# Optimization experiments

Measured on AMD Instinct MI355X. Metric: run time of the kernel, lower is better.

The kernel has to match this reference:

```python
import jax, jax.numpy as jnp
import numpy as np

CL = 128   # context_length
IL = 64    # inst_length
PC = 256; CH1 = 256; CH2 = 256; CH3 = 256
CK1 = 3; CK2 = 3; CK3 = 3
F1 = 512; OUT = 1
F1_INPUT = CH3 * (CL - 1 - CK1 - CK2 - CK3 + 3)  # 256*121 = 30976
B = 2048


def _conv1d(x, w, b):
    # x: [B, Cin, L], w: [Cout, Cin, K] -> [B, Cout, L-K+1]
    y = jax.lax.conv_general_dilated(x, w, window_strides=(1,), padding='VALID',
                                     dimension_numbers=('NCH', 'OIH', 'NCH'))
    return y + b[None, :, None]


def setup_inputs() -> dict:
    key = jax.random.key(0)
    ks = jax.random.split(key, 13)
    def w(k, shape, fan_in):
        bound = 1.0 / np.sqrt(fan_in)
        return jax.random.uniform(k, shape, jnp.float32, -bound, bound)
    return {
        'x':   jax.random.normal(ks[0], (B, CL * IL), jnp.float32),
        'Wp':  w(ks[1], (PC, IL, 2), IL * 2),
        'bp':  w(ks[2], (PC,), IL * 2),
        'W1':  w(ks[3], (CH1, PC, CK1), PC * CK1),
        'b1':  w(ks[4], (CH1,), PC * CK1),
        'W2':  w(ks[5], (CH2, CH1, CK2), CH1 * CK2),
        'b2':  w(ks[6], (CH2,), CH1 * CK2),
        'W3':  w(ks[7], (CH3, CH2, CK3), CH2 * CK3),
        'b3':  w(ks[8], (CH3,), CH2 * CK3),
        'Wf1': w(ks[9], (F1, F1_INPUT), F1_INPUT),
        'bf1': w(ks[10], (F1,), F1_INPUT),
        'Wf2': w(ks[11], (OUT, F1), F1),
        'bf2': w(ks[12], (OUT,), F1),
    }


def reference(x, Wp, bp, W1, b1, W2, b2, W3, b3, Wf1, bf1, Wf2, bf2):
    # [B, CL*IL] -> [B, IL, CL]
    xt = x.reshape(-1, CL, IL).transpose(0, 2, 1)
    # Fused pairwise convp: the torch loop computes, for i in 1..CL-1,
    #   y[:, c, i-1] = sum_j Wp[c,j,0]*x[:,j,0] + Wp[c,j,1]*x[:,j,i] + bp[c]
    x0 = xt[:, :, 0]          # [B, IL]
    xr = xt[:, :, 1:]         # [B, IL, CL-1]
    y = (jnp.einsum('bj,cj->bc', x0, Wp[:, :, 0])[:, :, None]
         + jnp.einsum('bjl,cj->bcl', xr, Wp[:, :, 1])
         + bp[None, :, None])                       # [B, PC, CL-1]
    h = jax.nn.relu(y)
    h = jax.nn.relu(_conv1d(h, W1, b1))
    h = jax.nn.relu(_conv1d(h, W2, b2))
    h = jax.nn.relu(_conv1d(h, W3, b3))
    h = h.reshape(-1, F1_INPUT)
    h = jax.nn.relu(h @ Wf1.T + bf1)
    return h @ Wf2.T + bf2    # [B, OUT]
```

## Files before the change

kernel.cpp:

```cpp
#include <hip/hip_runtime.h>

typedef _Float16 f16;
typedef _Float16 f16x8 __attribute__((ext_vector_type(8)));
typedef _Float16 f16x4 __attribute__((ext_vector_type(4)));
typedef float    f32x4 __attribute__((ext_vector_type(4)));

#define B_SZ   2048
#define NCH    256
#define L0_    127
#define L1_    125
#define L2_    123
#define L3_    121
#define F1_    512
#define FCK    30976
#define FCK2   31744
#define SPLIT  16
#define KPS2   62
#define NS_FC  31
#define BUFF   16384

__device__ __forceinline__ void gl16(const f16* g, f16* l) {
    __builtin_amdgcn_global_load_lds(
        (const __attribute__((address_space(1))) void*)g,
        (__attribute__((address_space(3))) void*)l, 16, 0, 0);
}

__global__ __launch_bounds__(256) void prep_w(const float* __restrict__ Wp,
                                              const float* __restrict__ W1,
                                              const float* __restrict__ W2,
                                              const float* __restrict__ W3,
                                              f16* __restrict__ wpw,
                                              f16* __restrict__ wct1,
                                              f16* __restrict__ wct2,
                                              f16* __restrict__ wct3) {
    int g = blockIdx.x;
    if (g < 128) {
        int idx = g * 256 + threadIdx.x;
        int ck = idx >> 13, co = (idx >> 5) & 255, w5 = idx & 31;
        int j = ck * 32 + w5;
        float v = (j < 64) ? Wp[co * 128 + j * 2 + 1]
                           : Wp[co * 128 + (j - 64) * 2];
        wpw[idx] = (f16)v;
        return;
    }
    int g2 = g - 128;
    const float* W = (g2 < 768) ? W1 : (g2 < 1536) ? W2 : W3;
    f16* dst = (g2 < 768) ? wct1 : (g2 < 1536) ? wct2 : wct3;
    int idx = (g2 % 768) * 256 + threadIdx.x;
    int ck = idx >> 13, co = (idx >> 5) & 255, w5 = idx & 31;
    int kt = ck * 32 + w5;
    int k = kt >> 8, ci = kt & 255;
    dst[idx] = (f16)W[((size_t)co * NCH + ci) * 3 + k];
}

__global__ __launch_bounds__(256) void prep_wf1k(const float* __restrict__ Wf1,
                                                 f16* __restrict__ wf1h) {
    __shared__ f16 t[NCH * 122];
    const int f = blockIdx.x, tid = threadIdx.x;
    const float* src = Wf1 + (size_t)f * FCK;
    for (int idx = tid; idx < FCK; idx += 256) {
        int co = idx / 121, l = idx - co * 121;
        t[co * 122 + l] = (f16)src[idx];
    }
    __syncthreads();
    f16* dst = wf1h + (size_t)f * FCK2;
    for (int idx = tid; idx < FCK2; idx += 256) {
        int l = idx >> 8, co = idx & 255;
        dst[idx] = (l < 121) ? t[co * 122 + l] : (f16)0.f;
    }
}

#define STAGEB(WT, S2, BUF)                                                   \
  {                                                                           \
    const f16* src0_ = (WT) + (size_t)(2 * (S2)) * 8192;                      \
    _Pragma("unroll")                                                         \
    for (int j = 0; j < 8; ++j) {                                             \
        int u_ = j * 256 + w * 64 + lane;                                     \
        int row_ = u_ >> 2, cu_ = u_ & 3;                                     \
        int cs_ = cu_ ^ ((row_ >> 2) & 3);                                    \
        gl16(src0_ + row_ * 32 + cs_ * 8,                                     \
             wlds + (BUF) * BUFF + (size_t)(j * 256 + w * 64) * 8);           \
    }                                                                         \
  }

#define GEMM_LAYER(WT, NS, CSTEPS)                                            \
  _Pragma("unroll")                                                           \
  for (int m = 0; m < 8; ++m)                                                 \
    _Pragma("unroll")                                                         \
    for (int n = 0; n < 4; ++n) acc[m][n] = (f32x4){0.f, 0.f, 0.f, 0.f};      \
  _Pragma("unroll 1")                                                         \
  for (int s = 0; s < (NS); ++s) {                                            \
    const int cur = s & 1;                                                    \
    if (s + 1 < (NS)) STAGEB(WT, s + 1, cur ^ 1)                              \
    __builtin_amdgcn_sched_barrier(0);                                        \
    _Pragma("unroll")                                                         \
    for (int kk = 0; kk < 2; ++kk) {                                          \
      const int ks32 = 2 * s + kk;                                            \
      const int k = ks32 / (CSTEPS), cb = (ks32 % (CSTEPS)) * 4;              \
      f16x8 a[8], bf[4];                                                      \
      _Pragma("unroll")                                                       \
      for (int m = 0; m < 8; ++m) {                                           \
        const int r_ = 16 * m + lr + k;                                       \
        a[m] = *(const f16x8*)(ins + r_ * 256 + (((cb + lh) ^ (r_ & 7)) << 3)); \
      }                                                                       \
      _Pragma("unroll")                                                       \
      for (int n = 0; n < 4; ++n) {                                           \
        const int co = wc0 + 16 * n + lr;                                     \
        bf[n] = *(const f16x8*)(wlds + cur * BUFF + kk * 8192                 \
                                + (co * 4 + (lh ^ ((co >> 2) & 3))) * 8);     \
      }                                                                       \
      __builtin_amdgcn_s_setprio(1);                                          \
      _Pragma("unroll")                                                       \
      for (int n = 0; n < 4; ++n)                                             \
        _Pragma("unroll")                                                     \
        for (int m = 0; m < 8; ++m)                                           \
          acc[m][n] = __builtin_amdgcn_mfma_f32_16x16x32_f16(a[m], bf[n],     \
                                                             acc[m][n], 0, 0, 0); \
      __builtin_amdgcn_s_setprio(0);                                          \
    }                                                                         \
    __builtin_amdgcn_sched_barrier(0);                                        \
    asm volatile("s_waitcnt vmcnt(0)" ::: "memory");                          \
    __builtin_amdgcn_sched_barrier(0);                                        \
    __builtin_amdgcn_s_barrier();                                             \
  }

#define EPI_LDS(BIAS, LOUT)                                                   \
  {                                                                           \
    _Pragma("unroll")                                                         \
    for (int n = 0; n < 4; ++n) {                                             \
      const int co = wc0 + 16 * n + lr;                                       \
      const float e = (BIAS)[co];                                             \
      const int sl = co >> 3, el = co & 7;                                    \
      _Pragma("unroll")                                                       \
      for (int m = 0; m < 8; ++m)                                             \
        _Pragma("unroll")                                                     \
        for (int r = 0; r < 4; ++r) {                                         \
          const int l = 16 * m + lh * 4 + r;                                  \
          if (l < (LOUT)) {                                                   \
            float v = fmaxf(acc[m][n][r] + e, 0.f);                           \
            ins[l * 256 + (((sl) ^ (l & 7)) << 3) + el] = (f16)v;             \
          }                                                                   \
        }                                                                     \
    }                                                                         \
  }

__global__ __launch_bounds__(256, 1) void fused_conv(
        const float* __restrict__ xin,
        const f16* __restrict__ wpw,  const float* __restrict__ bp,
        const f16* __restrict__ wct1, const float* __restrict__ b1,
        const f16* __restrict__ wct2, const float* __restrict__ b2,
        const f16* __restrict__ wct3, const float* __restrict__ b3,
        f16* __restrict__ h3out) {
    __shared__ f16 ins[130 * 256];
    __shared__ f16 wlds[2 * BUFF];

    const int b    = blockIdx.x;
    const int tid  = threadIdx.x;
    const int lane = tid & 63, w = tid >> 6;
    const int wc0  = w * 64;
    const int lr   = lane & 15, lh = lane >> 4;

    f32x4 acc[8][4];

    STAGEB(wpw, 0, 0)
    {
        const float* xr = xin + (size_t)b * 8192;
        for (int u = tid; u < 130 * 16; u += 256) {
            int r = u >> 4, sl = u & 15;
            int off = (sl < 8)
                ? ((r + 1 < 128 ? (r + 1) * 64 : 127 * 64) + sl * 8)
                : (sl - 8) * 8;
            float4 v0 = *(const float4*)(xr + off);
            float4 v1 = *(const float4*)(xr + off + 4);
            f16x8 h = { (f16)v0.x, (f16)v0.y, (f16)v0.z, (f16)v0.w,
                        (f16)v1.x, (f16)v1.y, (f16)v1.z, (f16)v1.w };
            *(f16x8*)(ins + r * 256 + ((sl ^ (r & 7)) << 3)) = h;
        }
    }
    __syncthreads();

    GEMM_LAYER(wpw, 2, 4)
    STAGEB(wct1, 0, 0)
    EPI_LDS(bp, L0_)
    asm volatile("s_waitcnt vmcnt(0) lgkmcnt(0)" ::: "memory");
    __builtin_amdgcn_s_barrier();

    GEMM_LAYER(wct1, 12, 8)
    STAGEB(wct2, 0, 0)
    EPI_LDS(b1, L1_)
    asm volatile("s_waitcnt vmcnt(0) lgkmcnt(0)" ::: "memory");
    __builtin_amdgcn_s_barrier();

    GEMM_LAYER(wct2, 12, 8)
    STAGEB(wct3, 0, 0)
    EPI_LDS(b2, L2_)
    asm volatile("s_waitcnt vmcnt(0) lgkmcnt(0)" ::: "memory");
    __builtin_amdgcn_s_barrier();

    GEMM_LAYER(wct3, 12, 8)
    EPI_LDS(b3, L3_)
    asm volatile("s_waitcnt lgkmcnt(0)" ::: "memory");
    __builtin_amdgcn_s_barrier();
    {
        f16* ob = h3out + (size_t)b * FCK2;
        const f16x8 z = { (f16)0.f, (f16)0.f, (f16)0.f, (f16)0.f,
                          (f16)0.f, (f16)0.f, (f16)0.f, (f16)0.f };
        for (int u = tid; u < 124 * 32; u += 256) {
            int r = u >> 5, sl = u & 31;
            f16x8 v = (r < L3_)
                ? *(const f16x8*)(ins + r * 256 + ((sl ^ (r & 7)) << 3))
                : z;
            *(f16x8*)(ob + r * 256 + sl * 8) = v;
        }
    }
}

__global__ __launch_bounds__(512, 1) void fc1k(const f16* __restrict__ A,
                                               const f16* __restrict__ Bw,
                                               float* __restrict__ part,
                                               int CB) {
    __shared__ f16 Asl[2 * 8192];
    __shared__ f16 Bsl[2 * 16384];
    const int m0 = blockIdx.x * 128, n0 = blockIdx.y * 256, sp = blockIdx.z;
    const int tid  = threadIdx.x;
    const int lane = tid & 63, w = tid >> 6;
    const int wb0  = (w >> 2) * 64, wf0 = (w & 3) * 64;
    const int lr   = lane & 15, lh = lane >> 4;
    const int ck0  = sp * KPS2;

    auto stage = [&](int s2, int buf) {
        const int k0 = (ck0 + 2 * s2) * 32;
#pragma unroll
        for (int j = 0; j < 2; ++j) {
            int u = j * 512 + tid;
            int row = u >> 3, cu = u & 7;
            int cs = cu ^ (row & 7);
            gl16(A + (size_t)(m0 + row) * FCK2 + k0 + cs * 8,
                 Asl + buf * 8192 + (size_t)(j * 512 + w * 64) * 8);
        }
#pragma unroll
        for (int j = 0; j < 4; ++j) {
            int u = j * 512 + tid;
            int row = u >> 3, cu = u & 7;
            int cs = cu ^ (row & 7);
            gl16(Bw + (size_t)(n0 + row) * FCK2 + k0 + cs * 8,
                 Bsl + buf * 16384 + (size_t)(j * 512 + w * 64) * 8);
        }
    };

    f32x4 acc[4][4];
#pragma unroll
    for (int m = 0; m < 4; ++m)
#pragma unroll
        for (int n = 0; n < 4; ++n) acc[m][n] = (f32x4){0.f, 0.f, 0.f, 0.f};

    stage(0, 0);
    __syncthreads();

#pragma unroll 1
    for (int s = 0; s < NS_FC; ++s) {
        const int cur = s & 1;
        if (s + 1 < NS_FC) stage(s + 1, cur ^ 1);
        __builtin_amdgcn_sched_barrier(0);
#pragma unroll
        for (int kk = 0; kk < 2; ++kk) {
            f16x8 a[4], bf[4];
#pragma unroll
            for (int m = 0; m < 4; ++m) {
                const int row = wb0 + 16 * m + lr;
                const int un = (kk * 4 + lh) ^ (row & 7);
                a[m] = *(const f16x8*)(Asl + cur * 8192 + row * 64 + un * 8);
            }
#pragma unroll
            for (int n = 0; n < 4; ++n) {
                const int row = wf0 + 16 * n + lr;
                const int un = (kk * 4 + lh) ^ (row & 7);
                bf[n] = *(const f16x8*)(Bsl + cur * 16384 + row * 64 + un * 8);
            }
            __builtin_amdgcn_s_setprio(1);
#pragma unroll
            for (int m = 0; m < 4; ++m)
#pragma unroll
                for (int n = 0; n < 4; ++n)
                    acc[m][n] = __builtin_amdgcn_mfma_f32_16x16x32_f16(
                        a[m], bf[n], acc[m][n], 0, 0, 0);
            __builtin_amdgcn_s_setprio(0);
        }
        __builtin_amdgcn_sched_barrier(0);
        asm volatile("s_waitcnt vmcnt(0)" ::: "memory");
        __builtin_amdgcn_sched_barrier(0);
        __builtin_amdgcn_s_barrier();
    }

#pragma unroll
    for (int m = 0; m < 4; ++m)
#pragma unroll
        for (int n = 0; n < 4; ++n)
#pragma unroll
            for (int r = 0; r < 4; ++r) {
                const int bl = m0 + wb0 + 16 * m + lh * 4 + r;
                const int f  = n0 + wf0 + 16 * n + lr;
                part[((size_t)sp * CB + bl) * F1_ + f] = acc[m][n][r];
            }
}

__global__ __launch_bounds__(512) void fcout(const float* __restrict__ part,
                                             const float* __restrict__ bf1,
                                             const float* __restrict__ Wf2,
                                             const float* __restrict__ bf2,
                                             float* __restrict__ out,
                                             int CB) {
    __shared__ float red[8];
    const int m = blockIdx.x;
    const int f = threadIdx.x;
    float s = bf1[f];
#pragma unroll
    for (int sp = 0; sp < SPLIT; ++sp)
        s += part[((size_t)sp * CB + m) * F1_ + f];
    float p = fmaxf(s, 0.f) * Wf2[f];
#pragma unroll
    for (int o = 32; o > 0; o >>= 1) p += __shfl_xor(p, o);
    if ((f & 63) == 0) red[f >> 6] = p;
    __syncthreads();
    if (f < 8) {
        float v = red[f];
        v += __shfl_xor(v, 1);
        v += __shfl_xor(v, 2);
        v += __shfl_xor(v, 4);
        if (f == 0) out[m] = v + bf2[0];
    }
}

extern "C" void kernel_launch(void* const* d_in, const int* in_sizes, int n_in,
                              void* d_out, int out_size, void* d_ws, size_t ws_size,
                              hipStream_t stream) {
    const float* x   = (const float*)d_in[0];
    const float* Wp  = (const float*)d_in[1];
    const float* bp  = (const float*)d_in[2];
    const float* W1  = (const float*)d_in[3];
    const float* b1  = (const float*)d_in[4];
    const float* W2  = (const float*)d_in[5];
    const float* b2  = (const float*)d_in[6];
    const float* W3  = (const float*)d_in[7];
    const float* b3  = (const float*)d_in[8];
    const float* Wf1 = (const float*)d_in[9];
    const float* bf1 = (const float*)d_in[10];
    const float* Wf2 = (const float*)d_in[11];
    const float* bf2 = (const float*)d_in[12];
    float* out = (float*)d_out;

    char* base = (char*)d_ws;
    size_t off = 0;
    auto alloc = [&](size_t bytes) {
        size_t o = off; off = (off + bytes + 255) & ~(size_t)255; return o;
    };
    const size_t o_wpw  = alloc((size_t)NCH * 128 * 2);
    const size_t o_wct1 = alloc((size_t)NCH * 768 * 2);
    const size_t o_wct2 = alloc((size_t)NCH * 768 * 2);
    const size_t o_wct3 = alloc((size_t)NCH * 768 * 2);
    const size_t o_wf1h = alloc((size_t)F1_ * FCK2 * 2);
    const size_t fixed  = off;

    int CB = 0;
    const int cand[5] = {2048, 1024, 512, 256, 128};
    for (int i = 0; i < 5; ++i) {
        size_t c = (size_t)cand[i];
        size_t need = fixed
            + (((size_t)SPLIT * c * F1_ * 4 + 255) & ~(size_t)255)
            + ((c * (size_t)FCK2 * 2 + 255) & ~(size_t)255);
        if (need <= ws_size) { CB = cand[i]; break; }
    }
    if (CB == 0) return;
    const int nchunk = B_SZ / CB;

    const size_t o_part = alloc((size_t)SPLIT * CB * F1_ * 4);
    const size_t o_h3   = alloc((size_t)CB * FCK2 * 2);

    f16*   wpw  = (f16*)(base + o_wpw);
    f16*   wct1 = (f16*)(base + o_wct1);
    f16*   wct2 = (f16*)(base + o_wct2);
    f16*   wct3 = (f16*)(base + o_wct3);
    f16*   wf1h = (f16*)(base + o_wf1h);
    float* part = (float*)(base + o_part);
    f16*   h3   = (f16*)(base + o_h3);

    prep_w<<<2432, 256, 0, stream>>>(Wp, W1, W2, W3, wpw, wct1, wct2, wct3);
    prep_wf1k<<<F1_, 256, 0, stream>>>(Wf1, wf1h);

    for (int c = 0; c < nchunk; ++c) {
        const size_t b0 = (size_t)c * CB;
        fused_conv<<<CB, 256, 0, stream>>>(x + b0 * 8192,
                                           wpw, bp, wct1, b1, wct2, b2,
                                           wct3, b3, h3);
        fc1k<<<dim3(CB / 128, 2, SPLIT), 512, 0, stream>>>(h3, wf1h, part, CB);
        fcout<<<CB, 512, 0, stream>>>(part, bf1, Wf2, bf2, out + b0, CB);
    }
}
```

Measured before the change: 631.1 us.

## Switch conv weight staging to triple-buffered single-kstep pipeline with partial vmcnt waits

Weight staging into LDS moves from double buffers holding two 32-wide k-steps to three buffers holding one k-step each. Loads are issued two steps ahead and gated with partial s_waitcnt vmcnt counts instead of draining all loads every iteration. Layer boundaries now prefetch the next layer's first two k-steps before the epilogue. This keeps more global loads in flight and shortens the serialized wait, at the cost of twice as many loop iterations and barriers per layer.

```diff
diff --git a/kernel.cpp b/kernel.cpp
--- a/kernel.cpp
+++ b/kernel.cpp
@@ -17,7 +17,7 @@
 #define SPLIT  16
 #define KPS2   62
 #define NS_FC  31
-#define BUFF   16384
+#define CBUF   8192
 
 __device__ __forceinline__ void gl16(const f16* g, f16* l) {
     __builtin_amdgcn_global_load_lds(
@@ -70,18 +70,14 @@
     }
 }
 
-#define STAGEB(WT, S2, BUF)                                                   \
-  {                                                                           \
-    const f16* src0_ = (WT) + (size_t)(2 * (S2)) * 8192;                      \
+#define STAGEC(WT, KS, BUF)                                                   \
+  { const f16* s0_ = (WT) + (size_t)(KS) * 8192;                              \
     _Pragma("unroll")                                                         \
-    for (int j = 0; j < 8; ++j) {                                             \
-        int u_ = j * 256 + w * 64 + lane;                                     \
-        int row_ = u_ >> 2, cu_ = u_ & 3;                                     \
-        int cs_ = cu_ ^ ((row_ >> 2) & 3);                                    \
-        gl16(src0_ + row_ * 32 + cs_ * 8,                                     \
-             wlds + (BUF) * BUFF + (size_t)(j * 256 + w * 64) * 8);           \
-    }                                                                         \
-  }
+    for (int j = 0; j < 4; ++j) {                                             \
+      int u_ = j * 256 + tid;                                                 \
+      int r_ = u_ >> 2, c_ = u_ & 3, cs_ = c_ ^ ((r_ >> 2) & 3);              \
+      gl16(s0_ + r_ * 32 + cs_ * 8,                                           \
+           wlds + (BUF) * CBUF + (size_t)(j * 256 + w * 64) * 8); } }
 
 #define GEMM_LAYER(WT, NS, CSTEPS)                                            \
   _Pragma("unroll")                                                           \
@@ -90,13 +86,21 @@
     for (int n = 0; n < 4; ++n) acc[m][n] = (f32x4){0.f, 0.f, 0.f, 0.f};      \
   _Pragma("unroll 1")                                                         \
   for (int s = 0; s < (NS); ++s) {                                            \
-    const int cur = s & 1;                                                    \
-    if (s + 1 < (NS)) STAGEB(WT, s + 1, cur ^ 1)                              \
+    const int cur = s % 3;                                                    \
+    if (s + 2 < (NS)) {                                                       \
+        STAGEC(WT, s + 2, (s + 2) % 3)                                        \
+        __builtin_amdgcn_sched_barrier(0);                                    \
+        asm volatile("s_waitcnt vmcnt(8)" ::: "memory");                      \
+    } else if (s + 1 < (NS)) {                                                \
+        asm volatile("s_waitcnt vmcnt(4)" ::: "memory");                      \
+    } else {                                                                  \
+        asm volatile("s_waitcnt vmcnt(0)" ::: "memory");                      \
+    }                                                                         \
     __builtin_amdgcn_sched_barrier(0);                                        \
-    _Pragma("unroll")                                                         \
-    for (int kk = 0; kk < 2; ++kk) {                                          \
-      const int ks32 = 2 * s + kk;                                            \
-      const int k = ks32 / (CSTEPS), cb = (ks32 % (CSTEPS)) * 4;              \
+    __builtin_amdgcn_s_barrier();                                             \
+    __builtin_amdgcn_sched_barrier(0);                                        \
+    {                                                                         \
+      const int k = s / (CSTEPS), cb = (s % (CSTEPS)) * 4;                    \
       f16x8 a[8], bf[4];                                                      \
       _Pragma("unroll")                                                       \
       for (int m = 0; m < 8; ++m) {                                           \
@@ -106,7 +110,7 @@
       _Pragma("unroll")                                                       \
       for (int n = 0; n < 4; ++n) {                                           \
         const int co = wc0 + 16 * n + lr;                                     \
-        bf[n] = *(const f16x8*)(wlds + cur * BUFF + kk * 8192                 \
+        bf[n] = *(const f16x8*)(wlds + cur * CBUF                             \
                                 + (co * 4 + (lh ^ ((co >> 2) & 3))) * 8);     \
       }                                                                       \
       __builtin_amdgcn_s_setprio(1);                                          \
@@ -118,8 +122,6 @@
                                                              acc[m][n], 0, 0, 0); \
       __builtin_amdgcn_s_setprio(0);                                          \
     }                                                                         \
-    __builtin_amdgcn_sched_barrier(0);                                        \
-    asm volatile("s_waitcnt vmcnt(0)" ::: "memory");                          \
     __builtin_amdgcn_sched_barrier(0);                                        \
     __builtin_amdgcn_s_barrier();                                             \
   }
@@ -144,6 +146,16 @@
     }                                                                         \
   }
 
+#define BOUNDARY(BIAS, LOUT, NEXTWT)                                          \
+  STAGEC(NEXTWT, 0, 0)                                                        \
+  STAGEC(NEXTWT, 1, 1)                                                        \
+  __builtin_amdgcn_sched_barrier(0);                                          \
+  EPI_LDS(BIAS, LOUT)                                                         \
+  __builtin_amdgcn_sched_barrier(0);                                          \
+  asm volatile("s_waitcnt lgkmcnt(0)" ::: "memory");                          \
+  __builtin_amdgcn_s_barrier();                                               \
+  __builtin_amdgcn_sched_barrier(0);
+
 __global__ __launch_bounds__(256, 1) void fused_conv(
         const float* __restrict__ xin,
         const f16* __restrict__ wpw,  const float* __restrict__ bp,
@@ -152,7 +164,7 @@
         const f16* __restrict__ wct3, const float* __restrict__ b3,
         f16* __restrict__ h3out) {
     __shared__ f16 ins[130 * 256];
-    __shared__ f16 wlds[2 * BUFF];
+    __shared__ f16 wlds[3 * CBUF];
 
     const int b    = blockIdx.x;
     const int tid  = threadIdx.x;
@@ -162,7 +174,8 @@
 
     f32x4 acc[8][4];
 
-    STAGEB(wpw, 0, 0)
+    STAGEC(wpw, 0, 0)
+    STAGEC(wpw, 1, 1)
     {
         const float* xr = xin + (size_t)b * 8192;
         for (int u = tid; u < 130 * 16; u += 256) {
@@ -179,25 +192,16 @@
     }
     __syncthreads();
 
-    GEMM_LAYER(wpw, 2, 4)
-    STAGEB(wct1, 0, 0)
-    EPI_LDS(bp, L0_)
-    asm volatile("s_waitcnt vmcnt(0) lgkmcnt(0)" ::: "memory");
-    __builtin_amdgcn_s_barrier();
-
-    GEMM_LAYER(wct1, 12, 8)
-    STAGEB(wct2, 0, 0)
-    EPI_LDS(b1, L1_)
-    asm volatile("s_waitcnt vmcnt(0) lgkmcnt(0)" ::: "memory");
-    __builtin_amdgcn_s_barrier();
-
-    GEMM_LAYER(wct2, 12, 8)
-    STAGEB(wct3, 0, 0)
-    EPI_LDS(b2, L2_)
-    asm volatile("s_waitcnt vmcnt(0) lgkmcnt(0)" ::: "memory");
-    __builtin_amdgcn_s_barrier();
-
-    GEMM_LAYER(wct3, 12, 8)
+    GEMM_LAYER(wpw, 4, 4)
+    BOUNDARY(bp, L0_, wct1)
+
+    GEMM_LAYER(wct1, 24, 8)
+    BOUNDARY(b1, L1_, wct2)
+
+    GEMM_LAYER(wct2, 24, 8)
+    BOUNDARY(b2, L2_, wct3)
+
+    GEMM_LAYER(wct3, 24, 8)
     EPI_LDS(b3, L3_)
     asm volatile("s_waitcnt lgkmcnt(0)" ::: "memory");
     __builtin_amdgcn_s_barrier();
```

Measured after the change: 688.6 us. 9.1% more time.
